# Kernel optimization log

Measured on AMD Instinct MI355X. Metric: run time of the kernel, lower is better.

The kernel has to match this reference:

```python
import jax, jax.numpy as jnp
import numpy as np

N, M = 8192, 128
EPS = 1e-4


def setup_inputs() -> dict:
    key = jax.random.key(0)
    k1, k2, k3 = jax.random.split(key, 3)
    out1 = jax.random.normal(k1, (N, M), dtype=jnp.float32)
    out2 = jax.random.normal(k2, (N, M), dtype=jnp.float32)
    label = jax.random.uniform(k3, (N, N), dtype=jnp.float32)
    return {"out1": out1, "out2": out2, "label": label}


def _dir_loss(a, b, mob):
    # pairwise_inner_product(a, b) in the torch code equals b @ a.T:
    # inner[i, j] = <b[i], a[j]>
    scores = jnp.einsum('im,jm->ij', b, a)          # [n, n]
    phat = jax.nn.softmax(scores, axis=-1)
    return jnp.sum(-mob * jnp.log(phat + EPS))


def reference(out1, out2, label):
    loss = _dir_loss(out1, out2, label)
    loss = loss + _dir_loss(out2, out1, label.T)
    return loss
```

## Files before the change

### kernel.cpp

```cpp
#include <hip/hip_runtime.h>
#include <hip/hip_bf16.h>
#include <stdint.h>

#define NN 8192
#define MM 128
#define EPSF 1e-4f
#define SHIFT 30.0f

typedef __bf16 bf16x8 __attribute__((ext_vector_type(8)));
typedef float floatx4 __attribute__((ext_vector_type(4)));

__device__ __forceinline__ void pf16(const float* g, void* lds) {
    __builtin_amdgcn_global_load_lds(
        (__attribute__((address_space(1))) void*)(uintptr_t)g,
        (__attribute__((address_space(3))) void*)(uint32_t)(uintptr_t)lds,
        16, 0, 0);
}

#define CVT8(dst, ptr)                                                        \
    do {                                                                      \
        float4 v0_ = *reinterpret_cast<const float4*>(ptr);                   \
        float4 v1_ = *reinterpret_cast<const float4*>((ptr) + 4);             \
        bf16x8 t_ = { (__bf16)v0_.x, (__bf16)v0_.y, (__bf16)v0_.z,            \
                      (__bf16)v0_.w, (__bf16)v1_.x, (__bf16)v1_.y,            \
                      (__bf16)v1_.z, (__bf16)v1_.w };                         \
        dst = t_;                                                             \
    } while (0)

__global__ __launch_bounds__(256)
void sums_kernel(const float* __restrict__ A, const float* __restrict__ B,
                 const float* __restrict__ label, float* __restrict__ sums) {
    __shared__ alignas(16) __bf16 Bs[2][64 * 128];
    __shared__ alignas(16) char pfbuf[1024];
    const int tid = threadIdx.x;
    const int w = tid >> 6, lane = tid & 63, q = lane >> 4, ln = lane & 15;
    const int i0 = blockIdx.y * 128 + w * 32;
    const int jbase = blockIdx.x * 512;
    const int bid = blockIdx.y * gridDim.x + blockIdx.x;
    const float* pfb = label + (size_t)NN * NN / 2 + (size_t)bid * 32768
                       + w * 1024 + lane * 4;

    const floatx4 accInit = {-SHIFT, -SHIFT, -SHIFT, -SHIFT};

    bf16x8 a[2][4];
    #pragma unroll
    for (int rg = 0; rg < 2; ++rg) {
        const float* ap = A + (size_t)(i0 + rg * 16 + ln) * MM + q * 8;
        #pragma unroll
        for (int k = 0; k < 4; ++k)
            CVT8(a[rg][k], ap + k * 32);
    }

#define STAGE(dstbuf, js_)                                                    \
    do {                                                                      \
        const float* srcb_ = B + (size_t)(jbase + (js_) * 64) * MM;           \
        char* d_ = reinterpret_cast<char*>(dstbuf);                           \
        _Pragma("unroll")                                                     \
        for (int u_ = 0; u_ < 4; ++u_) {                                      \
            int ch_ = u_ * 256 + tid;                                         \
            int row_ = ch_ >> 4, slot_ = ch_ & 15;                            \
            bf16x8 t2_;                                                       \
            CVT8(t2_, srcb_ + row_ * MM + slot_ * 8);                         \
            *reinterpret_cast<bf16x8*>(                                       \
                d_ + row_ * 256 + ((slot_ ^ (row_ & 7)) << 4)) = t2_;         \
        }                                                                     \
    } while (0)

    float p[2][4] = {{0.f, 0.f, 0.f, 0.f}, {0.f, 0.f, 0.f, 0.f}};

    STAGE(Bs[0], 0);
    int buf = 0;
    for (int js = 0; js < 8; ++js) {
        __syncthreads();
        #pragma unroll
        for (int u = 0; u < 4; ++u)
            pf16(pfb + js * 4096 + u * 256, pfbuf);
        if (js < 7) STAGE(Bs[buf ^ 1], js + 1);

        const int j0 = jbase + js * 64;
        const char* bsc = reinterpret_cast<const char*>(Bs[buf]);
        const int sw = ln & 7;
        #pragma unroll
        for (int cg = 0; cg < 4; ++cg) {
            const char* bp = bsc + (cg * 16 + ln) * 256;
            bf16x8 b[4];
            #pragma unroll
            for (int k = 0; k < 4; ++k)
                b[k] = *reinterpret_cast<const bf16x8*>(bp + (((q + 4 * k) ^ sw) << 4));
            floatx4 acc0 = accInit, acc1 = accInit;
            #pragma unroll
            for (int k = 0; k < 4; ++k) {
                acc0 = __builtin_amdgcn_mfma_f32_16x16x32_bf16(a[0][k], b[k], acc0, 0, 0, 0);
                acc1 = __builtin_amdgcn_mfma_f32_16x16x32_bf16(a[1][k], b[k], acc1, 0, 0, 0);
            }
            float e0[4], e1[4];
            #pragma unroll
            for (int r = 0; r < 4; ++r) {
                e0[r] = __expf(acc0[r]);
                e1[r] = __expf(acc1[r]);
                p[0][r] += e0[r];
                p[1][r] += e1[r];
            }
            float c = ((e0[0] + e0[1]) + (e0[2] + e0[3])) +
                      ((e1[0] + e1[1]) + (e1[2] + e1[3]));
            c += __shfl_xor(c, 16);
            c += __shfl_xor(c, 32);
            if (q == 0) atomicAdd(&sums[NN + j0 + cg * 16 + ln], c);
        }
        buf ^= 1;
    }
#undef STAGE

    #pragma unroll
    for (int m = 1; m <= 8; m <<= 1)
        #pragma unroll
        for (int rg = 0; rg < 2; ++rg)
            #pragma unroll
            for (int r = 0; r < 4; ++r)
                p[rg][r] += __shfl_xor(p[rg][r], m);
    if (ln == 0)
        #pragma unroll
        for (int rg = 0; rg < 2; ++rg)
            #pragma unroll
            for (int r = 0; r < 4; ++r)
                atomicAdd(&sums[i0 + rg * 16 + q * 4 + r], p[rg][r]);
}

__global__ __launch_bounds__(256)
void loss_kernel(const float* __restrict__ A, const float* __restrict__ B,
                 const float* __restrict__ sums, const float* __restrict__ label,
                 float* __restrict__ out) {
    __shared__ alignas(16) __bf16 Bs[128 * 128];
    __shared__ float Rr[128], Rc[128];
    __shared__ float red[4];
    const int tid = threadIdx.x;
    const int w = tid >> 6, lane = tid & 63, q = lane >> 4, ln = lane & 15;
    const int i0 = blockIdx.y * 128 + w * 32;
    const int jbase = blockIdx.x * 128;

    if (tid < 128) Rr[tid] = 1.0f / sums[blockIdx.y * 128 + tid];
    else           Rc[tid - 128] = 1.0f / sums[NN + jbase + (tid - 128)];

    {
        const float* srcb = B + (size_t)jbase * MM;
        char* d = reinterpret_cast<char*>(Bs);
        #pragma unroll
        for (int u = 0; u < 8; ++u) {
            int ch = u * 256 + tid;
            int row = ch >> 4, slot = ch & 15;
            bf16x8 t;
            CVT8(t, srcb + row * MM + slot * 8);
            *reinterpret_cast<bf16x8*>(d + row * 256 + ((slot ^ (row & 7)) << 4)) = t;
        }
    }

    const floatx4 accInit = {-SHIFT, -SHIFT, -SHIFT, -SHIFT};

    bf16x8 a[2][4];
    const float* labp[2];
    #pragma unroll
    for (int rg = 0; rg < 2; ++rg) {
        const int row = i0 + rg * 16 + ln;
        const float* ap = A + (size_t)row * MM + q * 8;
        #pragma unroll
        for (int k = 0; k < 4; ++k)
            CVT8(a[rg][k], ap + k * 32);
        labp[rg] = label + (size_t)row * NN;
    }
    __syncthreads();

    const float rl[2] = { Rr[w * 32 + ln], Rr[w * 32 + 16 + ln] };

    const char* bsc = reinterpret_cast<const char*>(Bs);
    const int sw = ln & 7;
    float lacc = 0.f;
    #pragma unroll
    for (int js = 0; js < 2; ++js) {
        const int j0 = js * 64;
        floatx4 rc[4], lb[2][4];
        #pragma unroll
        for (int cg = 0; cg < 4; ++cg) {
            const int c4 = j0 + cg * 16 + q * 4;
            rc[cg] = *reinterpret_cast<const floatx4*>(&Rc[c4]);
            lb[0][cg] = *reinterpret_cast<const floatx4*>(&labp[0][jbase + c4]);
            lb[1][cg] = *reinterpret_cast<const floatx4*>(&labp[1][jbase + c4]);
        }
        #pragma unroll
        for (int cg = 0; cg < 4; ++cg) {
            const char* bp = bsc + (j0 + cg * 16 + ln) * 256;
            bf16x8 b[4];
            #pragma unroll
            for (int k = 0; k < 4; ++k)
                b[k] = *reinterpret_cast<const bf16x8*>(bp + (((q + 4 * k) ^ sw) << 4));
            floatx4 acc0 = accInit, acc1 = accInit;
            #pragma unroll
            for (int k = 0; k < 4; ++k) {
                acc0 = __builtin_amdgcn_mfma_f32_16x16x32_bf16(b[k], a[0][k], acc0, 0, 0, 0);
                acc1 = __builtin_amdgcn_mfma_f32_16x16x32_bf16(b[k], a[1][k], acc1, 0, 0, 0);
            }
            #pragma unroll
            for (int r = 0; r < 4; ++r) {
                float e0 = __expf(acc0[r]);
                float t0 = __logf(fmaf(e0, rl[0], EPSF) * fmaf(e0, rc[cg][r], EPSF));
                lacc = fmaf(lb[0][cg][r], t0, lacc);
                float e1 = __expf(acc1[r]);
                float t1 = __logf(fmaf(e1, rl[1], EPSF) * fmaf(e1, rc[cg][r], EPSF));
                lacc = fmaf(lb[1][cg][r], t1, lacc);
            }
        }
    }

    #pragma unroll
    for (int m = 1; m <= 32; m <<= 1) lacc += __shfl_xor(lacc, m);
    if (lane == 0) red[w] = lacc;
    __syncthreads();
    if (tid == 0) atomicAdd(out, -((red[0] + red[1]) + (red[2] + red[3])));
}

extern "C" void kernel_launch(void* const* d_in, const int* in_sizes, int n_in,
                              void* d_out, int out_size, void* d_ws, size_t ws_size,
                              hipStream_t stream) {
    const float* out1 = (const float*)d_in[0];
    const float* out2 = (const float*)d_in[1];
    const float* label = (const float*)d_in[2];

    float* sums = (float*)d_ws;

    hipMemsetAsync(sums, 0, 2 * NN * sizeof(float), stream);
    hipMemsetAsync(d_out, 0, sizeof(float), stream);

    sums_kernel<<<dim3(16, 64), 256, 0, stream>>>(out2, out1, label, sums);

    loss_kernel<<<dim3(64, 64), 256, 0, stream>>>(out2, out1, sums, label,
                                                  (float*)d_out);
}
```

Measured before the change: 438.9 us.

## Retile sums kernel to 256x256 blocks, prefetch label's first half, fold out memset

The sums kernel now has each wave own 64 rows (four MFMA row groups) over a 256-column strip instead of 32 rows over 512 columns. This raises reuse of each staged B tile and halves the column-sum atomics per output. The L2 prefetch of label moves from the second half of the matrix to the first half with a new per-block layout. The separate memset of the output scalar is dropped and the output is zeroed inside the sums kernel instead. The cost is more accumulator registers and possibly lower occupancy.

```diff
diff --git a/kernel.cpp b/kernel.cpp
--- a/kernel.cpp
+++ b/kernel.cpp
@@ -29,22 +29,24 @@
 
 __global__ __launch_bounds__(256)
 void sums_kernel(const float* __restrict__ A, const float* __restrict__ B,
-                 const float* __restrict__ label, float* __restrict__ sums) {
+                 const float* __restrict__ label, float* __restrict__ sums,
+                 float* __restrict__ out) {
     __shared__ alignas(16) __bf16 Bs[2][64 * 128];
     __shared__ alignas(16) char pfbuf[1024];
     const int tid = threadIdx.x;
     const int w = tid >> 6, lane = tid & 63, q = lane >> 4, ln = lane & 15;
-    const int i0 = blockIdx.y * 128 + w * 32;
-    const int jbase = blockIdx.x * 512;
+    const int i0 = blockIdx.y * 256 + w * 64;
+    const int jbase = blockIdx.x * 256;
     const int bid = blockIdx.y * gridDim.x + blockIdx.x;
-    const float* pfb = label + (size_t)NN * NN / 2 + (size_t)bid * 32768
-                       + w * 1024 + lane * 4;
+    const float* pfb = label + (size_t)bid * 32768 + w * 8192 + lane * 4;
+
+    if (bid == 0 && tid == 0) *out = 0.f;
 
     const floatx4 accInit = {-SHIFT, -SHIFT, -SHIFT, -SHIFT};
 
-    bf16x8 a[2][4];
-    #pragma unroll
-    for (int rg = 0; rg < 2; ++rg) {
+    bf16x8 a[4][4];
+    #pragma unroll
+    for (int rg = 0; rg < 4; ++rg) {
         const float* ap = A + (size_t)(i0 + rg * 16 + ln) * MM + q * 8;
         #pragma unroll
         for (int k = 0; k < 4; ++k)
@@ -66,16 +68,20 @@
         }                                                                     \
     } while (0)
 
-    float p[2][4] = {{0.f, 0.f, 0.f, 0.f}, {0.f, 0.f, 0.f, 0.f}};
+    float p[4][4];
+    #pragma unroll
+    for (int rg = 0; rg < 4; ++rg)
+        #pragma unroll
+        for (int r = 0; r < 4; ++r) p[rg][r] = 0.f;
 
     STAGE(Bs[0], 0);
     int buf = 0;
-    for (int js = 0; js < 8; ++js) {
+    for (int js = 0; js < 4; ++js) {
         __syncthreads();
-        #pragma unroll
-        for (int u = 0; u < 4; ++u)
-            pf16(pfb + js * 4096 + u * 256, pfbuf);
-        if (js < 7) STAGE(Bs[buf ^ 1], js + 1);
+        if (js < 3) STAGE(Bs[buf ^ 1], js + 1);
+        #pragma unroll
+        for (int u = 0; u < 8; ++u)
+            pf16(pfb + js * 2048 + u * 256, pfbuf);
 
         const int j0 = jbase + js * 64;
         const char* bsc = reinterpret_cast<const char*>(Bs[buf]);
@@ -87,22 +93,23 @@
             #pragma unroll
             for (int k = 0; k < 4; ++k)
                 b[k] = *reinterpret_cast<const bf16x8*>(bp + (((q + 4 * k) ^ sw) << 4));
-            floatx4 acc0 = accInit, acc1 = accInit;
-            #pragma unroll
-            for (int k = 0; k < 4; ++k) {
-                acc0 = __builtin_amdgcn_mfma_f32_16x16x32_bf16(a[0][k], b[k], acc0, 0, 0, 0);
-                acc1 = __builtin_amdgcn_mfma_f32_16x16x32_bf16(a[1][k], b[k], acc1, 0, 0, 0);
+            floatx4 acc[4] = {accInit, accInit, accInit, accInit};
+            #pragma unroll
+            for (int k = 0; k < 4; ++k)
+                #pragma unroll
+                for (int rg = 0; rg < 4; ++rg)
+                    acc[rg] = __builtin_amdgcn_mfma_f32_16x16x32_bf16(a[rg][k], b[k], acc[rg], 0, 0, 0);
+            float c = 0.f;
+            #pragma unroll
+            for (int rg = 0; rg < 4; ++rg) {
+                float e[4];
+                #pragma unroll
+                for (int r = 0; r < 4; ++r) {
+                    e[r] = __expf(acc[rg][r]);
+                    p[rg][r] += e[r];
+                }
+                c += (e[0] + e[1]) + (e[2] + e[3]);
             }
-            float e0[4], e1[4];
-            #pragma unroll
-            for (int r = 0; r < 4; ++r) {
-                e0[r] = __expf(acc0[r]);
-                e1[r] = __expf(acc1[r]);
-                p[0][r] += e0[r];
-                p[1][r] += e1[r];
-            }
-            float c = ((e0[0] + e0[1]) + (e0[2] + e0[3])) +
-                      ((e1[0] + e1[1]) + (e1[2] + e1[3]));
             c += __shfl_xor(c, 16);
             c += __shfl_xor(c, 32);
             if (q == 0) atomicAdd(&sums[NN + j0 + cg * 16 + ln], c);
@@ -114,13 +121,13 @@
     #pragma unroll
     for (int m = 1; m <= 8; m <<= 1)
         #pragma unroll
-        for (int rg = 0; rg < 2; ++rg)
+        for (int rg = 0; rg < 4; ++rg)
             #pragma unroll
             for (int r = 0; r < 4; ++r)
                 p[rg][r] += __shfl_xor(p[rg][r], m);
     if (ln == 0)
         #pragma unroll
-        for (int rg = 0; rg < 2; ++rg)
+        for (int rg = 0; rg < 4; ++rg)
             #pragma unroll
             for (int r = 0; r < 4; ++r)
                 atomicAdd(&sums[i0 + rg * 16 + q * 4 + r], p[rg][r]);
@@ -227,9 +234,9 @@
     float* sums = (float*)d_ws;
 
     hipMemsetAsync(sums, 0, 2 * NN * sizeof(float), stream);
-    hipMemsetAsync(d_out, 0, sizeof(float), stream);
-
-    sums_kernel<<<dim3(16, 64), 256, 0, stream>>>(out2, out1, label, sums);
+
+    sums_kernel<<<dim3(32, 32), 256, 0, stream>>>(out2, out1, label, sums,
+                                                  (float*)d_out);
 
     loss_kernel<<<dim3(64, 64), 256, 0, stream>>>(out2, out1, sums, label,
                                                   (float*)d_out);
```

After: 432.6 us. About the same (-1.4%).
